# Optimization experiments

Measured on AMD Instinct MI355X. Metric: run time of the kernel, lower is better.

Reference implementation:

```python
import jax, jax.numpy as jnp
import numpy as np
from jax import lax

B, CODELEN, COMLEN, NAST, SUBG = 32, 50, 30, 300, 4
EMB, H, ASTHOPS = 300, 256, 2
AST_VOCAB, COM_VOCAB = 10000, 10000


def gru(x, h0, wih, whh, bih, bhh):
    # PyTorch GRU cell semantics. x: [N, T, D], h0: [N, H] -> (ys [N,T,H], hT [N,H])
    xg = jnp.einsum('ntd,gd->ntg', x, wih) + bih  # precompute input gates [N,T,3H]
    def step(h, xt):
        hg = h @ whh.T + bhh
        xr, xz, xn = jnp.split(xt, 3, axis=-1)
        hr, hz, hn = jnp.split(hg, 3, axis=-1)
        r = jax.nn.sigmoid(xr + hr)
        z = jax.nn.sigmoid(xz + hz)
        n = jnp.tanh(xn + r * hn)
        hnew = (1.0 - z) * n + z * h
        return hnew, hnew
    hT, ys = lax.scan(step, h0, jnp.swapaxes(xg, 0, 1))
    return jnp.swapaxes(ys, 0, 1), hT


def dot_attn(q, k):
    # DotProductAttention in eval mode (dropout = identity)
    scale = 1.0 / jnp.sqrt(jnp.asarray(q.shape[-1], q.dtype))
    s = jnp.einsum('bqd,bkd->bqk', q, k) * scale
    return jnp.einsum('bqk,bkd->bqd', jax.nn.softmax(s, axis=-1), k)


def setup_inputs() -> dict:
    key = jax.random.key(0)
    ks = jax.random.split(key, 32)
    def rn(k, shp, sc=0.05):
        return jax.random.normal(k, shp, jnp.float32) * sc
    inp = {}
    inp['x0'] = jax.random.randint(ks[0], (B, CODELEN), 0, AST_VOCAB)
    inp['x1'] = jax.random.randint(ks[1], (B, COMLEN), 0, COM_VOCAB)
    inp['x2'] = jax.random.randint(ks[2], (B, SUBG, NAST), 0, AST_VOCAB)
    inp['adj'] = jax.random.uniform(ks[3], (B, SUBG, NAST, NAST), jnp.float32) * (1.0 / NAST)
    inp['emb_ast'] = rn(ks[4], (AST_VOCAB, EMB), 0.5)
    inp['emb_com'] = rn(ks[5], (COM_VOCAB, EMB), 0.5)
    inp['gru1_wih'] = rn(ks[6], (3 * H, EMB)); inp['gru1_whh'] = rn(ks[7], (3 * H, H))
    inp['gru1_bih'] = rn(ks[8], (3 * H,));    inp['gru1_bhh'] = rn(ks[9], (3 * H,))
    inp['gru2_wih'] = rn(ks[10], (3 * H, EMB)); inp['gru2_whh'] = rn(ks[11], (3 * H, H))
    inp['gru2_bih'] = rn(ks[12], (3 * H,));     inp['gru2_bhh'] = rn(ks[13], (3 * H,))
    inp['gru4_wih'] = rn(ks[14], (3 * H, NAST * EMB), 0.01)
    inp['gru4_whh'] = rn(ks[15], (3 * H, H))
    inp['gru4_bih'] = rn(ks[16], (3 * H,)); inp['gru4_bhh'] = rn(ks[17], (3 * H,))
    inp['gru58_wih'] = rn(ks[18], (SUBG, 3 * H, EMB)); inp['gru58_whh'] = rn(ks[19], (SUBG, 3 * H, H))
    inp['gru58_bih'] = rn(ks[20], (SUBG, 3 * H));      inp['gru58_bhh'] = rn(ks[21], (SUBG, 3 * H))
    inp['gcn_w'] = rn(ks[22], (EMB, EMB)); inp['gcn_b'] = rn(ks[23], (EMB,))
    inp['dense_w'] = rn(ks[24], (H, 3 * H)); inp['dense_b'] = rn(ks[25], (H,))
    inp['lin_w'] = rn(ks[26], (COM_VOCAB, COMLEN * H), 0.01); inp['lin_b'] = rn(ks[27], (COM_VOCAB,))
    return inp


def reference(x0, x1, x2, adj, emb_ast, emb_com,
              gru1_wih, gru1_whh, gru1_bih, gru1_bhh,
              gru2_wih, gru2_whh, gru2_bih, gru2_bhh,
              gru4_wih, gru4_whh, gru4_bih, gru4_bhh,
              gru58_wih, gru58_whh, gru58_bih, gru58_bhh,
              gcn_w, gcn_b, dense_w, dense_b, lin_w, lin_b):
    b = x0.shape[0]
    scale = 1.0 / jnp.sqrt(jnp.float32(H))
    # token encoder + comment decoder
    tencout, tstate = gru(emb_ast[x0], jnp.zeros((b, H), jnp.float32),
                          gru1_wih, gru1_whh, gru1_bih, gru1_bhh)
    decout, _ = gru(emb_com[x1], tstate, gru2_wih, gru2_whh, gru2_bih, gru2_bhh)
    tcontext = dot_attn(decout, tencout)
    # GCN over 4 sub-graphs (torch code mutates astwork in place -> tmp alias sees post-GCN feats)
    astwork = jnp.transpose(emb_ast[x2], (1, 0, 2, 3))  # [4,B,N,300]
    adjp = jnp.transpose(adj, (1, 0, 2, 3))             # [4,B,N,N]
    for _ in range(ASTHOPS):
        support = jnp.einsum('sbnd,de->sbne', astwork, gcn_w)
        astwork = jax.nn.relu(jnp.einsum('sbnm,sbme->sbne', adjp, support) + gcn_b)
    # TimeDistributed(gru4): batch = 4 sub-graphs, sequence = B, input = flattened node feats
    g4in = astwork.reshape(SUBG, b, NAST * EMB)
    g4out, _ = gru(g4in, jnp.zeros((SUBG, H), jnp.float32),
                   gru4_wih, gru4_whh, gru4_bih, gru4_bhh)
    astw = jnp.transpose(g4out, (1, 0, 2))  # [B,4,H]
    ahier = jax.nn.softmax(jnp.einsum('bqd,bsd->bqs', decout, astw) * scale, axis=-1)
    ahier_p = jnp.transpose(ahier, (2, 0, 1))  # [4,B,Q]
    # per-sub-graph node GRUs (gru5..gru8) vmapped over the sub-graph axis
    outs, _ = jax.vmap(gru, in_axes=(0, None, 0, 0, 0, 0))(
        astwork, tstate, gru58_wih, gru58_whh, gru58_bih, gru58_bhh)  # [4,B,N,H]
    sc = jax.nn.softmax(jnp.einsum('bqd,sbkd->sbqk', decout, outs) * scale, axis=-1)
    new_atten = sc * ahier_p[:, :, :, None]  # element_wise_mul with hierarchy weights
    acontext = jnp.einsum('sbqk,sbkd->bqd', new_atten, outs)  # bmm then sum over sub-graphs
    acontext = dot_attn(decout, acontext)
    context = jnp.concatenate([tcontext, decout, acontext], axis=-1)  # [B,Q,768]
    out = jax.nn.relu(context @ dense_w.T + dense_b)
    out = out.reshape(b, -1)  # [B, 7680]
    return out @ lin_w.T + lin_b  # [B, comvocab]
```

## Files before the change

kernel.cpp:

```cpp
#include <hip/hip_runtime.h>
#include <hip/hip_fp16.h>
#include <hip/hip_bf16.h>


typedef __attribute__((ext_vector_type(8))) short  bf16x8;
typedef __attribute__((ext_vector_type(4))) float  f32x4;

__device__ inline unsigned short f2bs(float f) {
  __hip_bfloat16 h = __float2bfloat16(f);
  unsigned short u; __builtin_memcpy(&u, &h, 2); return u;
}
__device__ inline float bs2f(unsigned short u) {
  unsigned v = (unsigned)u << 16;
  float f; __builtin_memcpy(&f, &v, 4); return f;
}
__device__ inline float sigf(float x) { return 1.f / (1.f + __expf(-x)); }
__device__ inline float tanhf_(float x) {
  const float e = __expf(-2.f * fabsf(x));
  return copysignf((1.f - e) / (1.f + e), x);
}

template <bool ABF, bool BBF, int OUTM, bool RELU, bool GATHER = false, bool BKN = false>
__global__ __launch_bounds__(256) void k_mfma(
    const void* __restrict__ Av, long lda, long a_ss, long a_sb,
    const void* __restrict__ Bv, long ldb, long b_ss, long b_sb,
    void* __restrict__ Cv, long ldc, long c_ss, long c_sb,
    const float* __restrict__ bias, long bias_ss,
    const int* __restrict__ gidx,
    int M, int N, int K, int zb, int ksplit)
{
  __shared__ unsigned short As[128][40];
  __shared__ unsigned short Bs[128][40];
  const int tid = threadIdx.x;
  const int zi = blockIdx.z;
  const int bi = zi / ksplit;
  const int ks = zi - bi * ksplit;
  const int sIdx = bi / zb;
  const int bIdx = bi - sIdx * zb;
  const int row0 = blockIdx.y * 128;
  const int col0 = blockIdx.x * 128;
  const int Kc = ((K + ksplit * 32 - 1) / (ksplit * 32)) * 32;
  const int kbeg = ks * Kc;
  const int kend = min(K, kbeg + Kc);
  if (kbeg >= kend) return;

  const char* Ab = (const char*)Av + ((long)sIdx * a_ss + (long)bIdx * a_sb) * (ABF ? 2 : 4);
  const char* Bb = (const char*)Bv + ((long)sIdx * b_ss + (long)bIdx * b_sb) * (BBF ? 2 : 4);
  char* Cb = (char*)Cv + ((long)sIdx * c_ss + (long)bIdx * c_sb) * ((OUTM == 1 || OUTM == 3) ? 2 : 4);

  const int w = tid >> 6, l = tid & 63;
  const int wr = w >> 1, wc = w & 1;
  const int lr = l & 15, lg = l >> 4;

  f32x4 acc[4][4];
#pragma unroll
  for (int m = 0; m < 4; ++m)
#pragma unroll
    for (int n = 0; n < 4; ++n) acc[m][n] = f32x4{0.f, 0.f, 0.f, 0.f};

  const int sr = tid >> 1;
  const int sk = (tid & 1) * 16;

  for (int kt = kbeg; kt < kend; kt += 32) {
    {
      const int gr = row0 + sr;
      if (ABF) {
        const unsigned short* src = (const unsigned short*)(Ab + ((long)gr * lda + kt + sk) * 2);
        if (gr < M && kt + sk + 16 <= kend) {
          const uint2* p = (const uint2*)src;
          *(uint2*)&As[sr][sk + 0]  = p[0];
          *(uint2*)&As[sr][sk + 4]  = p[1];
          *(uint2*)&As[sr][sk + 8]  = p[2];
          *(uint2*)&As[sr][sk + 12] = p[3];
        } else {
#pragma unroll
          for (int i = 0; i < 16; ++i) {
            const int kk = kt + sk + i;
            As[sr][sk + i] = (gr < M && kk < kend) ? src[i] : (unsigned short)0;
          }
        }
      } else {
        const float* src;
        if (GATHER) src = (const float*)Av + ((gr < M) ? (long)gidx[gr] * lda : 0) + kt + sk;
        else        src = (const float*)(Ab + ((long)gr * lda + kt + sk) * 4);
        if (gr < M && kt + sk + 16 <= kend) {
#pragma unroll
          for (int q = 0; q < 4; ++q) {
            const float4 v = ((const float4*)src)[q];
            *(unsigned*)&As[sr][sk + q * 4 + 0] = (unsigned)f2bs(v.x) | ((unsigned)f2bs(v.y) << 16);
            *(unsigned*)&As[sr][sk + q * 4 + 2] = (unsigned)f2bs(v.z) | ((unsigned)f2bs(v.w) << 16);
          }
        } else {
#pragma unroll
          for (int i = 0; i < 16; ++i) {
            const int kk = kt + sk + i;
            As[sr][sk + i] = (gr < M && kk < kend) ? f2bs(src[i]) : (unsigned short)0;
          }
        }
      }
    }
    if (BKN) {
      const int kk = tid >> 3;
      const int cb = (tid & 7) * 16;
      const int gk = kt + kk;
#pragma unroll
      for (int q = 0; q < 16; ++q) {
        const int gc = col0 + cb + q;
        unsigned short v = 0;
        if (gk < kend && gc < N) {
          if (BBF) v = ((const unsigned short*)Bb)[(long)gk * ldb + gc];
          else     v = f2bs(((const float*)Bb)[(long)gk * ldb + gc]);
        }
        Bs[cb + q][kk] = v;
      }
    } else {
      const int gc = col0 + sr;
      if (BBF) {
        const unsigned short* src = (const unsigned short*)(Bb + ((long)gc * ldb + kt + sk) * 2);
        if (gc < N && kt + sk + 16 <= kend) {
          const uint2* p = (const uint2*)src;
          *(uint2*)&Bs[sr][sk + 0]  = p[0];
          *(uint2*)&Bs[sr][sk + 4]  = p[1];
          *(uint2*)&Bs[sr][sk + 8]  = p[2];
          *(uint2*)&Bs[sr][sk + 12] = p[3];
        } else {
#pragma unroll
          for (int i = 0; i < 16; ++i) {
            const int kk = kt + sk + i;
            Bs[sr][sk + i] = (gc < N && kk < kend) ? src[i] : (unsigned short)0;
          }
        }
      } else {
        const float* src = (const float*)(Bb + ((long)gc * ldb + kt + sk) * 4);
        if (gc < N && kt + sk + 16 <= kend) {
#pragma unroll
          for (int q = 0; q < 4; ++q) {
            const float4 v = ((const float4*)src)[q];
            *(unsigned*)&Bs[sr][sk + q * 4 + 0] = (unsigned)f2bs(v.x) | ((unsigned)f2bs(v.y) << 16);
            *(unsigned*)&Bs[sr][sk + q * 4 + 2] = (unsigned)f2bs(v.z) | ((unsigned)f2bs(v.w) << 16);
          }
        } else {
#pragma unroll
          for (int i = 0; i < 16; ++i) {
            const int kk = kt + sk + i;
            Bs[sr][sk + i] = (gc < N && kk < kend) ? f2bs(src[i]) : (unsigned short)0;
          }
        }
      }
    }
    __syncthreads();
    bf16x8 af[4], bf[4];
#pragma unroll
    for (int m = 0; m < 4; ++m)
      af[m] = *(const bf16x8*)&As[wr * 64 + m * 16 + lr][lg * 8];
#pragma unroll
    for (int n = 0; n < 4; ++n)
      bf[n] = *(const bf16x8*)&Bs[wc * 64 + n * 16 + lr][lg * 8];
#pragma unroll
    for (int m = 0; m < 4; ++m)
#pragma unroll
      for (int n = 0; n < 4; ++n)
        acc[m][n] = __builtin_amdgcn_mfma_f32_16x16x32_bf16(af[m], bf[n], acc[m][n], 0, 0, 0);
    __syncthreads();
  }

  const float* bp = bias ? bias + (long)sIdx * bias_ss : nullptr;
#pragma unroll
  for (int m = 0; m < 4; ++m) {
#pragma unroll
    for (int n = 0; n < 4; ++n) {
      const int col = col0 + wc * 64 + n * 16 + lr;
      const int rb  = row0 + wr * 64 + m * 16 + lg * 4;
      const f32x4 v = acc[m][n];
      if (col >= N) continue;
      if (OUTM == 3) {
        unsigned short* ct = (unsigned short*)Cb + (long)col * ldc + rb;
        if (rb + 4 <= M) {
          ushort4 pk;
          pk.x = f2bs(v[0]); pk.y = f2bs(v[1]); pk.z = f2bs(v[2]); pk.w = f2bs(v[3]);
          *(ushort4*)ct = pk;
        } else {
#pragma unroll
          for (int r = 0; r < 4; ++r) if (rb + r < M) ct[r] = f2bs(v[r]);
        }
      } else {
        const float bv = bp ? bp[col] : 0.f;
#pragma unroll
        for (int r = 0; r < 4; ++r) {
          const int row = rb + r;
          if (row >= M) continue;
          float x = v[r] + bv;
          if (RELU) x = fmaxf(x, 0.f);
          if (OUTM == 0) ((float*)Cb)[(long)row * ldc + col] = x;
          else if (OUTM == 1) ((unsigned short*)Cb)[(long)row * ldc + col] = f2bs(x);
          else atomicAdd((float*)Cb + (long)row * ldc + col, x);
        }
      }
    }
  }
}

template <int CPB, bool YBF>
__global__ __launch_bounds__(512, 2)
void k_gru_v6(
    const unsigned short* __restrict__ xg,
    const float* __restrict__ h0, int h0_mod,
    const unsigned short* __restrict__ whh_bf, long w_stride, int cpw,
    const float* __restrict__ bhh, long b_stride,
    void* __restrict__ ys, float* __restrict__ hT, int T)
{
  const int tid = threadIdx.x;
  const int c0  = blockIdx.x * CPB;
  const int wv  = tid >> 6;
  const int l   = tid & 63;
  const int lr  = l & 15;
  const int lg  = l >> 4;

  __shared__ unsigned short A_lds[512][8];
  __shared__ unsigned short w_lds[8][8][64][8];
  __shared__ float gate_lds[CPB][772];
  __shared__ float bhh_lds[768];

  const unsigned short* W = whh_bf + (long)(c0 / cpw) * w_stride;
  bf16x8 bfr[5][8];
#pragma unroll
  for (int nt = 0; nt < 5; ++nt) {
    const unsigned short* wp = W + (long)(wv * 96 + nt * 16 + lr) * 256 + lg * 8;
#pragma unroll
    for (int kt = 0; kt < 8; ++kt) bfr[nt][kt] = *(const bf16x8*)(wp + kt * 32);
  }
  {
    const unsigned short* wp = W + (long)(wv * 96 + 80 + lr) * 256 + lg * 8;
#pragma unroll
    for (int kt = 0; kt < 8; ++kt)
      *(bf16x8*)&w_lds[wv][kt][l][0] = *(const bf16x8*)(wp + kt * 32);
  }
  for (int i = tid; i < 768; i += 512)
    bhh_lds[i] = bhh[(long)(c0 / cpw) * b_stride + i];

  const bool act = lr < CPB;
  const int cO  = lr;
  const int u0  = wv * 32 + lg * 8;

  float h[8];
  {
    bf16x8 pk;
#pragma unroll
    for (int e = 0; e < 8; ++e) {
      float hv = 0.f;
      if (act && h0) hv = h0[(long)((c0 + cO) % h0_mod) * 256 + u0 + e];
      h[e] = hv;
      pk[e] = (short)f2bs(hv);
    }
    *(bf16x8*)&A_lds[tid][0] = pk;
  }

  const unsigned short* xrow = xg + (long)(c0 + cO) * T * 768 + u0;
  bf16x8 xv0, xv1, xv2;
  if (act) {
    xv0 = *(const bf16x8*)(xrow);
    xv1 = *(const bf16x8*)(xrow + 256);
    xv2 = *(const bf16x8*)(xrow + 512);
  }
  __syncthreads();

  for (int t = 0; t < T; ++t) {
    f32x4 acc[6];
#pragma unroll
    for (int nt = 0; nt < 6; ++nt) acc[nt] = f32x4{0.f, 0.f, 0.f, 0.f};
#pragma unroll
    for (int kt = 0; kt < 8; ++kt) {
      const bf16x8 af = *(const bf16x8*)&A_lds[kt * 64 + l][0];
#pragma unroll
      for (int nt = 0; nt < 5; ++nt)
        acc[nt] = __builtin_amdgcn_mfma_f32_16x16x32_bf16(af, bfr[nt][kt], acc[nt], 0, 0, 0);
      const bf16x8 wf = *(const bf16x8*)&w_lds[wv][kt][l][0];
      acc[5] = __builtin_amdgcn_mfma_f32_16x16x32_bf16(af, wf, acc[5], 0, 0, 0);
    }
    if (lg * 4 < CPB) {
#pragma unroll
      for (int nt = 0; nt < 6; ++nt) {
        const int col = wv * 96 + nt * 16 + lr;
#pragma unroll
        for (int r = 0; r < 4; ++r) gate_lds[lg * 4 + r][col] = acc[nt][r];
      }
    }
    asm volatile("s_waitcnt lgkmcnt(0)" ::: "memory");
    __builtin_amdgcn_sched_barrier(0);
    __builtin_amdgcn_s_barrier();
    __builtin_amdgcn_sched_barrier(0);

    if (act) {
      float xr[8], xz[8], xn[8];
#pragma unroll
      for (int e = 0; e < 8; ++e) {
        xr[e] = bs2f((unsigned short)xv0[e]);
        xz[e] = bs2f((unsigned short)xv1[e]);
        xn[e] = bs2f((unsigned short)xv2[e]);
      }
      bf16x8 pk;
#pragma unroll
      for (int e = 0; e < 8; ++e) {
        const int u = u0 + e;
        const float rr = sigf(xr[e] + gate_lds[cO][u] + bhh_lds[u]);
        const float zz = sigf(xz[e] + gate_lds[cO][256 + u] + bhh_lds[256 + u]);
        const float nv = tanhf_(xn[e] + rr * (gate_lds[cO][512 + u] + bhh_lds[512 + u]));
        h[e] = (1.f - zz) * nv + zz * h[e];
        pk[e] = (short)f2bs(h[e]);
      }
      *(bf16x8*)&A_lds[tid][0] = pk;
      if (YBF) {
        *(bf16x8*)((unsigned short*)ys + ((long)(c0 + cO) * T + t) * 256 + u0) = pk;
      } else {
        float* yp = (float*)ys + ((long)(c0 + cO) * T + t) * 256 + u0;
        *(float4*)yp = float4{h[0], h[1], h[2], h[3]};
        *(float4*)(yp + 4) = float4{h[4], h[5], h[6], h[7]};
      }
      if (t + 1 < T) {
        const unsigned short* xp = xrow + (long)(t + 1) * 768;
        xv0 = *(const bf16x8*)(xp);
        xv1 = *(const bf16x8*)(xp + 256);
        xv2 = *(const bf16x8*)(xp + 512);
      }
    }
    asm volatile("s_waitcnt lgkmcnt(0)" ::: "memory");
    __builtin_amdgcn_sched_barrier(0);
    __builtin_amdgcn_s_barrier();
    __builtin_amdgcn_sched_barrier(0);
  }
  if (act && hT) {
    float* hp = hT + (long)(c0 + cO) * 256 + u0;
    *(float4*)hp = float4{h[0], h[1], h[2], h[3]};
    *(float4*)(hp + 4) = float4{h[4], h[5], h[6], h[7]};
  }
}

__global__ __launch_bounds__(256) void k_init_bias(
    float* __restrict__ C, const float* __restrict__ bias, int M, int N)
{
  const int total = M * N;
  for (int i = blockIdx.x * 256 + threadIdx.x; i < total; i += gridDim.x * 256)
    C[i] = bias[i % N];
}

__global__ __launch_bounds__(256) void k_gather_ast(
    const float* __restrict__ emb, const int* __restrict__ x2,
    unsigned short* __restrict__ outp)
{
  const int total = 4 * 32 * 300 * 300;
  for (int idx = blockIdx.x * 256 + threadIdx.x; idx < total; idx += gridDim.x * 256) {
    const int d = idx % 300;
    const int r = idx / 300;
    const int n = r % 300;
    const int r2 = r / 300;
    const int b = r2 % 32;
    const int s = r2 / 32;
    outp[idx] = f2bs(emb[(long)x2[(b * 4 + s) * 300 + n] * 300 + d]);
  }
}

__global__ __launch_bounds__(256) void k_twb(
    const float* __restrict__ w, unsigned short* __restrict__ o, int R, int C)
{
  const int total = R * C;
  for (int i = blockIdx.x * 256 + threadIdx.x; i < total; i += gridDim.x * 256) {
    const int r = i / C, c = i - r * C;
    o[(long)c * R + r] = f2bs(w[i]);
  }
}

__global__ __launch_bounds__(256) void k_f2b(
    const float* __restrict__ a, unsigned short* __restrict__ o, int n)
{
  for (int i = blockIdx.x * 256 + threadIdx.x; i < n; i += gridDim.x * 256)
    o[i] = f2bs(a[i]);
}

__global__ __launch_bounds__(256) void k_attn(
    const float* __restrict__ q, const float* __restrict__ kv,
    float* __restrict__ out, int Q, int L)
{
  const int bq = blockIdx.x;
  const int b = bq / Q;
  const int tid = threadIdx.x;
  const int g = tid >> 3, l = tid & 7;
  __shared__ float qv[256];
  __shared__ float sc[64];
  qv[tid] = q[(long)bq * 256 + tid];
  __syncthreads();
  for (int k0 = 0; k0 < L; k0 += 32) {
    const int k = k0 + g;
    float s = 0.f;
    if (k < L) {
      const float* kr = kv + ((long)b * L + k) * 256;
      for (int d = l; d < 256; d += 8) s += qv[d] * kr[d];
    }
    s += __shfl_xor(s, 1);
    s += __shfl_xor(s, 2);
    s += __shfl_xor(s, 4);
    if (k < L && l == 0) sc[k] = s * 0.0625f;
  }
  __syncthreads();
  float m = -1e30f;
  for (int k = 0; k < L; ++k) m = fmaxf(m, sc[k]);
  float den = 0.f;
  for (int k = 0; k < L; ++k) den += __expf(sc[k] - m);
  __syncthreads();
  if (tid < L) sc[tid] = __expf(sc[tid] - m);
  __syncthreads();
  const float* kb = kv + (long)b * L * 256;
  float acc = 0.f;
  for (int k = 0; k < L; ++k) acc += sc[k] * kb[(long)k * 256 + tid];
  out[(long)bq * 256 + tid] = acc / den;
}

__global__ __launch_bounds__(64) void k_hier(
    const float* __restrict__ dec, const float* __restrict__ g4out,
    float* __restrict__ ahier, int Q)
{
  const int bq = blockIdx.x;
  const int b = bq / Q;
  const int l = threadIdx.x;
  float s[4] = {0.f, 0.f, 0.f, 0.f};
#pragma unroll
  for (int i = 0; i < 4; ++i) {
    const int d = l * 4 + i;
    const float qd = dec[(long)bq * 256 + d];
#pragma unroll
    for (int sg = 0; sg < 4; ++sg)
      s[sg] += qd * g4out[((long)sg * 32 + b) * 256 + d];
  }
#pragma unroll
  for (int off = 32; off >= 1; off >>= 1)
#pragma unroll
    for (int sg = 0; sg < 4; ++sg) s[sg] += __shfl_xor(s[sg], off);
  if (l == 0) {
    float m = -1e30f;
#pragma unroll
    for (int sg = 0; sg < 4; ++sg) m = fmaxf(m, s[sg] * 0.0625f);
    float e[4], den = 0.f;
#pragma unroll
    for (int sg = 0; sg < 4; ++sg) { e[sg] = __expf(s[sg] * 0.0625f - m); den += e[sg]; }
#pragma unroll
    for (int sg = 0; sg < 4; ++sg) ahier[(long)bq * 4 + sg] = e[sg] / den;
  }
}

__global__ __launch_bounds__(64) void k_smax(
    float* __restrict__ sc, const float* __restrict__ ahier)
{
  const int id = blockIdx.x;
  const int s = id / 960;
  const int bq = id - s * 960;
  float* row = sc + (long)id * 300;
  const int l = threadIdx.x;
  float v[5];
  float m = -1e30f;
#pragma unroll
  for (int i = 0; i < 5; ++i) {
    const int k = l + i * 64;
    v[i] = (k < 300) ? row[k] * 0.0625f : -1e30f;
    m = fmaxf(m, v[i]);
  }
#pragma unroll
  for (int off = 32; off >= 1; off >>= 1) m = fmaxf(m, __shfl_xor(m, off));
  float den = 0.f;
#pragma unroll
  for (int i = 0; i < 5; ++i) { v[i] = __expf(v[i] - m); den += v[i]; }
#pragma unroll
  for (int off = 32; off >= 1; off >>= 1) den += __shfl_xor(den, off);
  const float w = ahier[(long)bq * 4 + s] / den;
#pragma unroll
  for (int i = 0; i < 5; ++i) {
    const int k = l + i * 64;
    if (k < 300) row[k] = v[i] * w;
  }
}

__global__ __launch_bounds__(256) void k_concat(
    const float* __restrict__ a, const float* __restrict__ b,
    const float* __restrict__ c, float* __restrict__ out, int rows)
{
  const int total = rows * 768;
  for (int i = blockIdx.x * 256 + threadIdx.x; i < total; i += gridDim.x * 256) {
    const int r = i / 768, col = i - r * 768;
    float v;
    if (col < 256) v = a[(long)r * 256 + col];
    else if (col < 512) v = b[(long)r * 256 + col - 256];
    else v = c[(long)r * 256 + col - 512];
    out[i] = v;
  }
}

extern "C" void kernel_launch(void* const* d_in, const int* in_sizes, int n_in,
                              void* d_out, int out_size, void* d_ws, size_t ws_size,
                              hipStream_t stream) {
  const int*   x0      = (const int*)d_in[0];
  const int*   x1      = (const int*)d_in[1];
  const int*   x2      = (const int*)d_in[2];
  const float* adj     = (const float*)d_in[3];
  const float* emb_ast = (const float*)d_in[4];
  const float* emb_com = (const float*)d_in[5];
  const float* g1_wih  = (const float*)d_in[6];
  const float* g1_whh  = (const float*)d_in[7];
  const float* g1_bih  = (const float*)d_in[8];
  const float* g1_bhh  = (const float*)d_in[9];
  const float* g2_wih  = (const float*)d_in[10];
  const float* g2_whh  = (const float*)d_in[11];
  const float* g2_bih  = (const float*)d_in[12];
  const float* g2_bhh  = (const float*)d_in[13];
  const float* g4_wih  = (const float*)d_in[14];
  const float* g4_whh  = (const float*)d_in[15];
  const float* g4_bih  = (const float*)d_in[16];
  const float* g4_bhh  = (const float*)d_in[17];
  const float* g58_wih = (const float*)d_in[18];
  const float* g58_whh = (const float*)d_in[19];
  const float* g58_bih = (const float*)d_in[20];
  const float* g58_bhh = (const float*)d_in[21];
  const float* gcn_w   = (const float*)d_in[22];
  const float* gcn_b   = (const float*)d_in[23];
  const float* dw      = (const float*)d_in[24];
  const float* db      = (const float*)d_in[25];
  const float* lw      = (const float*)d_in[26];
  const float* lb      = (const float*)d_in[27];
  float* out = (float*)d_out;
  float* ws  = (float*)d_ws;

  unsigned short* astwork_bf = (unsigned short*)ws;
  unsigned short* supportT   = (unsigned short*)(ws + 5760000L);
  unsigned short* g58xg_bf   = (unsigned short*)(ws + 11520000L);
  unsigned short* outsb_bf   = (unsigned short*)(ws + 26265600L);
  unsigned short* xg1_bf     = (unsigned short*)(ws + 31180800L);
  unsigned short* xg2_bf     = (unsigned short*)(ws + 31795200L);
  float* tenc    = ws + 32163840L;
  float* tstate  = ws + 32573440L;
  float* dec     = ws + 32581632L;
  float* tctx    = ws + 32827392L;
  float* g4xg    = ws + 33073152L;
  float* g4out   = ws + 33171456L;
  float* ahier   = ws + 33204224L;
  float* actx1   = ws + 33208064L;
  float* actx    = ws + 33453824L;
  float* dense   = ws + 33699584L;
  float* ctmp    = ws + 33945344L;
  float* scbuf   = ws + 34682624L;
  unsigned short* gcn_wT    = (unsigned short*)(ws + 35834624L);
  unsigned short* dense_bf  = (unsigned short*)(ws + 35879624L);
  unsigned short* g1whh_bf  = (unsigned short*)(ws + 36002504L);
  unsigned short* g2whh_bf  = (unsigned short*)(ws + 36100808L);
  unsigned short* g4whh_bf  = (unsigned short*)(ws + 36199112L);
  unsigned short* g58whh_bf = (unsigned short*)(ws + 36297416L);
  unsigned short* adj_bf    = (unsigned short*)(ws + 36690632L);
  unsigned short* g4xg_bf   = (unsigned short*)(ws + 42450632L);

  const dim3 blk(256);

  k_gather_ast<<<dim3(4096), blk, 0, stream>>>(emb_ast, x2, astwork_bf);
  k_twb<<<dim3(90), blk, 0, stream>>>(gcn_w, gcn_wT, 300, 300);
  k_f2b<<<dim3(192), blk, 0, stream>>>(g1_whh, g1whh_bf, 196608);
  k_f2b<<<dim3(192), blk, 0, stream>>>(g2_whh, g2whh_bf, 196608);
  k_f2b<<<dim3(192), blk, 0, stream>>>(g4_whh, g4whh_bf, 196608);
  k_f2b<<<dim3(768), blk, 0, stream>>>(g58_whh, g58whh_bf, 786432);
  k_f2b<<<dim3(4096), blk, 0, stream>>>(adj, adj_bf, 11520000);

  for (int hop = 0; hop < 2; ++hop) {
    k_mfma<true, true, 3, false><<<dim3(3, 3, 128), blk, 0, stream>>>(
        astwork_bf, 300, 2880000, 90000,
        gcn_wT, 300, 0, 0,
        supportT, 300, 2880000, 90000,
        nullptr, 0, nullptr, 300, 300, 300, 32, 1);
    k_mfma<true, true, 1, true><<<dim3(3, 3, 128), blk, 0, stream>>>(
        adj_bf, 300, 90000, 360000,
        supportT, 300, 2880000, 90000,
        astwork_bf, 300, 2880000, 90000,
        gcn_b, 0, nullptr, 300, 300, 300, 32, 1);
  }

  k_mfma<false, false, 1, false, true><<<dim3(6, 13, 1), blk, 0, stream>>>(
      emb_ast, 300, 0, 0, g1_wih, 300, 0, 0, xg1_bf, 768, 0, 0,
      g1_bih, 0, x0, 1600, 768, 300, 1, 1);
  k_gru_v6<8, false><<<dim3(4), dim3(512), 0, stream>>>(
      xg1_bf, nullptr, 1, g1whh_bf, 0, 32, g1_bhh, 0, tenc, tstate, 50);

  k_mfma<false, false, 1, false, true><<<dim3(6, 8, 1), blk, 0, stream>>>(
      emb_com, 300, 0, 0, g2_wih, 300, 0, 0, xg2_bf, 768, 0, 0,
      g2_bih, 0, x1, 960, 768, 300, 1, 1);
  k_gru_v6<8, false><<<dim3(4), dim3(512), 0, stream>>>(
      xg2_bf, tstate, 32, g2whh_bf, 0, 32, g2_bhh, 0, dec, nullptr, 30);

  k_attn<<<dim3(960), blk, 0, stream>>>(dec, tenc, tctx, 30, 50);

  k_init_bias<<<dim3(384), blk, 0, stream>>>(g4xg, g4_bih, 128, 768);
  k_mfma<true, false, 2, false><<<dim3(6, 1, 43), blk, 0, stream>>>(
      astwork_bf, 90000, 0, 0, g4_wih, 90000, 0, 0, g4xg, 768, 0, 0,
      nullptr, 0, nullptr, 128, 768, 90000, 1, 43);
  k_f2b<<<dim3(384), blk, 0, stream>>>(g4xg, g4xg_bf, 98304);
  k_gru_v6<4, false><<<dim3(1), dim3(512), 0, stream>>>(
      g4xg_bf, nullptr, 1, g4whh_bf, 0, 4, g4_bhh, 0, g4out, nullptr, 32);

  k_hier<<<dim3(960), dim3(64), 0, stream>>>(dec, g4out, ahier, 30);

  k_mfma<true, false, 1, false><<<dim3(6, 75, 4), blk, 0, stream>>>(
      astwork_bf, 300, 2880000, 0, g58_wih, 300, 230400, 0,
      g58xg_bf, 768, 7372800, 0, g58_bih, 768, nullptr, 9600, 768, 300, 1, 1);
  k_gru_v6<8, true><<<dim3(16), dim3(512), 0, stream>>>(
      g58xg_bf, tstate, 32, g58whh_bf, 196608, 32, g58_bhh, 768,
      outsb_bf, nullptr, 300);

  k_mfma<false, true, 0, false><<<dim3(3, 1, 128), blk, 0, stream>>>(
      dec, 256, 0, 7680, outsb_bf, 256, 2457600, 76800, scbuf, 300, 288000, 9000,
      nullptr, 0, nullptr, 30, 300, 256, 32, 1);
  k_smax<<<dim3(3840), dim3(64), 0, stream>>>(scbuf, ahier);
  hipMemsetAsync(actx1, 0, 245760 * sizeof(float), stream);
  k_mfma<false, true, 2, false, false, true><<<dim3(2, 1, 128), blk, 0, stream>>>(
      scbuf, 300, 288000, 9000, outsb_bf, 256, 2457600, 76800, actx1, 256, 0, 7680,
      nullptr, 0, nullptr, 30, 256, 300, 32, 1);

  k_attn<<<dim3(960), blk, 0, stream>>>(dec, actx1, actx, 30, 30);

  k_concat<<<dim3(2880), blk, 0, stream>>>(tctx, dec, actx, ctmp, 960);
  k_mfma<false, false, 0, true><<<dim3(2, 8, 1), blk, 0, stream>>>(
      ctmp, 768, 0, 0, dw, 768, 0, 0, dense, 256, 0, 0,
      db, 0, nullptr, 960, 256, 768, 1, 1);
  k_f2b<<<dim3(960), blk, 0, stream>>>(dense, dense_bf, 245760);

  k_init_bias<<<dim3(1250), blk, 0, stream>>>(out, lb, 32, 10000);
  k_mfma<true, false, 2, false><<<dim3(79, 1, 6), blk, 0, stream>>>(
      dense_bf, 7680, 0, 0, lw, 7680, 0, 0, out, 10000, 0, 0,
      nullptr, 0, nullptr, 32, 10000, 7680, 1, 6);
}
```

Measured before the change: 2.104 ms.

## Replace MFMA batched GRU with one-sequence-per-block fp16 register GRU

Replaces the GRU recurrence kernel, which batched 8 sequences per block with MFMA and bf16 weights, with one sequence per 1024-thread block. Each thread keeps its share of the fp16-packed recurrent weights in registers and computes dot products with packed half2 FMAs, then reduces across 4 lanes with shuffles. This spreads the serial recurrences over many more CUs (128 blocks for the 300-step sub-graph GRU) and drops the separate weight-conversion kernels. The cost is fp16 accumulation in short partial sums, which loses some precision, and heavy register pressure from 96 half2 weight registers per thread.

```diff
diff --git a/kernel.cpp b/kernel.cpp
--- a/kernel.cpp
+++ b/kernel.cpp
@@ -200,139 +200,101 @@
   }
 }
 
-template <int CPB, bool YBF>
-__global__ __launch_bounds__(512, 2)
-void k_gru_v6(
+template <bool YBF>
+__global__ __launch_bounds__(1024) void k_gru_v7(
     const unsigned short* __restrict__ xg,
     const float* __restrict__ h0, int h0_mod,
-    const unsigned short* __restrict__ whh_bf, long w_stride, int cpw,
+    const float* __restrict__ whh, long w_stride, int cpw,
     const float* __restrict__ bhh, long b_stride,
     void* __restrict__ ys, float* __restrict__ hT, int T)
 {
+  const int c   = blockIdx.x;
   const int tid = threadIdx.x;
-  const int c0  = blockIdx.x * CPB;
-  const int wv  = tid >> 6;
-  const int l   = tid & 63;
-  const int lr  = l & 15;
-  const int lg  = l >> 4;
-
-  __shared__ unsigned short A_lds[512][8];
-  __shared__ unsigned short w_lds[8][8][64][8];
-  __shared__ float gate_lds[CPB][772];
-  __shared__ float bhh_lds[768];
-
-  const unsigned short* W = whh_bf + (long)(c0 / cpw) * w_stride;
-  bf16x8 bfr[5][8];
-#pragma unroll
-  for (int nt = 0; nt < 5; ++nt) {
-    const unsigned short* wp = W + (long)(wv * 96 + nt * 16 + lr) * 256 + lg * 8;
-#pragma unroll
-    for (int kt = 0; kt < 8; ++kt) bfr[nt][kt] = *(const bf16x8*)(wp + kt * 32);
-  }
+  const int j   = tid >> 2;
+  const int kq  = tid & 3;
+
+  __shared__ __half h16[256];
+
+  const float* W = whh + (long)(c / cpw) * w_stride;
+  __half2 wr[32], wz[32], wn[32];
   {
-    const unsigned short* wp = W + (long)(wv * 96 + 80 + lr) * 256 + lg * 8;
-#pragma unroll
-    for (int kt = 0; kt < 8; ++kt)
-      *(bf16x8*)&w_lds[wv][kt][l][0] = *(const bf16x8*)(wp + kt * 32);
-  }
-  for (int i = tid; i < 768; i += 512)
-    bhh_lds[i] = bhh[(long)(c0 / cpw) * b_stride + i];
-
-  const bool act = lr < CPB;
-  const int cO  = lr;
-  const int u0  = wv * 32 + lg * 8;
-
-  float h[8];
-  {
-    bf16x8 pk;
-#pragma unroll
-    for (int e = 0; e < 8; ++e) {
-      float hv = 0.f;
-      if (act && h0) hv = h0[(long)((c0 + cO) % h0_mod) * 256 + u0 + e];
-      h[e] = hv;
-      pk[e] = (short)f2bs(hv);
-    }
-    *(bf16x8*)&A_lds[tid][0] = pk;
-  }
-
-  const unsigned short* xrow = xg + (long)(c0 + cO) * T * 768 + u0;
-  bf16x8 xv0, xv1, xv2;
+    const float* pr = W + (long)j * 256 + kq * 64;
+    const float* pz = W + (long)(j + 256) * 256 + kq * 64;
+    const float* pn = W + (long)(j + 512) * 256 + kq * 64;
+#pragma unroll
+    for (int i = 0; i < 32; ++i) {
+      wr[i] = __floats2half2_rn(pr[2 * i], pr[2 * i + 1]);
+      wz[i] = __floats2half2_rn(pz[2 * i], pz[2 * i + 1]);
+      wn[i] = __floats2half2_rn(pn[2 * i], pn[2 * i + 1]);
+    }
+  }
+
+  const bool act = (kq == 0);
+  float br = 0.f, bz = 0.f, bn = 0.f, hold = 0.f;
   if (act) {
-    xv0 = *(const bf16x8*)(xrow);
-    xv1 = *(const bf16x8*)(xrow + 256);
-    xv2 = *(const bf16x8*)(xrow + 512);
-  }
-  __syncthreads();
+    const float* Bh = bhh + (long)(c / cpw) * b_stride;
+    br = Bh[j]; bz = Bh[256 + j]; bn = Bh[512 + j];
+    hold = h0 ? h0[(long)(c % h0_mod) * 256 + j] : 0.f;
+    h16[j] = __float2half(hold);
+  }
+  const unsigned short* xrow = xg + (long)c * T * 768;
+  float xr = 0.f, xz = 0.f, xn = 0.f;
+  if (act) {
+    xr = bs2f(xrow[j]); xz = bs2f(xrow[256 + j]); xn = bs2f(xrow[512 + j]);
+  }
+  asm volatile("s_waitcnt lgkmcnt(0)" ::: "memory");
+  __builtin_amdgcn_sched_barrier(0);
+  __builtin_amdgcn_s_barrier();
+  __builtin_amdgcn_sched_barrier(0);
 
   for (int t = 0; t < T; ++t) {
-    f32x4 acc[6];
-#pragma unroll
-    for (int nt = 0; nt < 6; ++nt) acc[nt] = f32x4{0.f, 0.f, 0.f, 0.f};
-#pragma unroll
-    for (int kt = 0; kt < 8; ++kt) {
-      const bf16x8 af = *(const bf16x8*)&A_lds[kt * 64 + l][0];
-#pragma unroll
-      for (int nt = 0; nt < 5; ++nt)
-        acc[nt] = __builtin_amdgcn_mfma_f32_16x16x32_bf16(af, bfr[nt][kt], acc[nt], 0, 0, 0);
-      const bf16x8 wf = *(const bf16x8*)&w_lds[wv][kt][l][0];
-      acc[5] = __builtin_amdgcn_mfma_f32_16x16x32_bf16(af, wf, acc[5], 0, 0, 0);
-    }
-    if (lg * 4 < CPB) {
-#pragma unroll
-      for (int nt = 0; nt < 6; ++nt) {
-        const int col = wv * 96 + nt * 16 + lr;
-#pragma unroll
-        for (int r = 0; r < 4; ++r) gate_lds[lg * 4 + r][col] = acc[nt][r];
+    float nxr = 0.f, nxz = 0.f, nxn = 0.f;
+    if (act && t + 1 < T) {
+      const unsigned short* xp = xrow + (long)(t + 1) * 768;
+      nxr = bs2f(xp[j]); nxz = bs2f(xp[256 + j]); nxn = bs2f(xp[512 + j]);
+    }
+    const __half2* hp = (const __half2*)&h16[0] + kq * 32;
+    float sr = 0.f, sz = 0.f, sn = 0.f;
+#pragma unroll
+    for (int i0 = 0; i0 < 32; i0 += 8) {
+      __half2 ar = __float2half2_rn(0.f);
+      __half2 az = __float2half2_rn(0.f);
+      __half2 an = __float2half2_rn(0.f);
+#pragma unroll
+      for (int i = 0; i < 8; ++i) {
+        const __half2 hv = hp[i0 + i];
+        ar = __hfma2(wr[i0 + i], hv, ar);
+        az = __hfma2(wz[i0 + i], hv, az);
+        an = __hfma2(wn[i0 + i], hv, an);
       }
-    }
+      sr += __low2float(ar) + __high2float(ar);
+      sz += __low2float(az) + __high2float(az);
+      sn += __low2float(an) + __high2float(an);
+    }
+    sr += __shfl_xor(sr, 1); sr += __shfl_xor(sr, 2);
+    sz += __shfl_xor(sz, 1); sz += __shfl_xor(sz, 2);
+    sn += __shfl_xor(sn, 1); sn += __shfl_xor(sn, 2);
     asm volatile("s_waitcnt lgkmcnt(0)" ::: "memory");
     __builtin_amdgcn_sched_barrier(0);
     __builtin_amdgcn_s_barrier();
     __builtin_amdgcn_sched_barrier(0);
 
     if (act) {
-      float xr[8], xz[8], xn[8];
-#pragma unroll
-      for (int e = 0; e < 8; ++e) {
-        xr[e] = bs2f((unsigned short)xv0[e]);
-        xz[e] = bs2f((unsigned short)xv1[e]);
-        xn[e] = bs2f((unsigned short)xv2[e]);
-      }
-      bf16x8 pk;
-#pragma unroll
-      for (int e = 0; e < 8; ++e) {
-        const int u = u0 + e;
-        const float rr = sigf(xr[e] + gate_lds[cO][u] + bhh_lds[u]);
-        const float zz = sigf(xz[e] + gate_lds[cO][256 + u] + bhh_lds[256 + u]);
-        const float nv = tanhf_(xn[e] + rr * (gate_lds[cO][512 + u] + bhh_lds[512 + u]));
-        h[e] = (1.f - zz) * nv + zz * h[e];
-        pk[e] = (short)f2bs(h[e]);
-      }
-      *(bf16x8*)&A_lds[tid][0] = pk;
-      if (YBF) {
-        *(bf16x8*)((unsigned short*)ys + ((long)(c0 + cO) * T + t) * 256 + u0) = pk;
-      } else {
-        float* yp = (float*)ys + ((long)(c0 + cO) * T + t) * 256 + u0;
-        *(float4*)yp = float4{h[0], h[1], h[2], h[3]};
-        *(float4*)(yp + 4) = float4{h[4], h[5], h[6], h[7]};
-      }
-      if (t + 1 < T) {
-        const unsigned short* xp = xrow + (long)(t + 1) * 768;
-        xv0 = *(const bf16x8*)(xp);
-        xv1 = *(const bf16x8*)(xp + 256);
-        xv2 = *(const bf16x8*)(xp + 512);
-      }
-    }
+      const float rr = sigf(xr + sr + br);
+      const float zz = sigf(xz + sz + bz);
+      const float nv = tanhf_(xn + rr * (sn + bn));
+      hold = (1.f - zz) * nv + zz * hold;
+      h16[j] = __float2half(hold);
+      if (YBF) ((unsigned short*)ys)[((long)c * T + t) * 256 + j] = f2bs(hold);
+      else     ((float*)ys)[((long)c * T + t) * 256 + j] = hold;
+    }
+    xr = nxr; xz = nxz; xn = nxn;
     asm volatile("s_waitcnt lgkmcnt(0)" ::: "memory");
     __builtin_amdgcn_sched_barrier(0);
     __builtin_amdgcn_s_barrier();
     __builtin_amdgcn_sched_barrier(0);
   }
-  if (act && hT) {
-    float* hp = hT + (long)(c0 + cO) * 256 + u0;
-    *(float4*)hp = float4{h[0], h[1], h[2], h[3]};
-    *(float4*)(hp + 4) = float4{h[4], h[5], h[6], h[7]};
-  }
+  if (act && hT) hT[(long)c * 256 + j] = hold;
 }
 
 __global__ __launch_bounds__(256) void k_init_bias(
@@ -546,10 +508,6 @@
   float* scbuf   = ws + 34682624L;
   unsigned short* gcn_wT    = (unsigned short*)(ws + 35834624L);
   unsigned short* dense_bf  = (unsigned short*)(ws + 35879624L);
-  unsigned short* g1whh_bf  = (unsigned short*)(ws + 36002504L);
-  unsigned short* g2whh_bf  = (unsigned short*)(ws + 36100808L);
-  unsigned short* g4whh_bf  = (unsigned short*)(ws + 36199112L);
-  unsigned short* g58whh_bf = (unsigned short*)(ws + 36297416L);
   unsigned short* adj_bf    = (unsigned short*)(ws + 36690632L);
   unsigned short* g4xg_bf   = (unsigned short*)(ws + 42450632L);
 
@@ -557,10 +515,6 @@
 
   k_gather_ast<<<dim3(4096), blk, 0, stream>>>(emb_ast, x2, astwork_bf);
   k_twb<<<dim3(90), blk, 0, stream>>>(gcn_w, gcn_wT, 300, 300);
-  k_f2b<<<dim3(192), blk, 0, stream>>>(g1_whh, g1whh_bf, 196608);
-  k_f2b<<<dim3(192), blk, 0, stream>>>(g2_whh, g2whh_bf, 196608);
-  k_f2b<<<dim3(192), blk, 0, stream>>>(g4_whh, g4whh_bf, 196608);
-  k_f2b<<<dim3(768), blk, 0, stream>>>(g58_whh, g58whh_bf, 786432);
   k_f2b<<<dim3(4096), blk, 0, stream>>>(adj, adj_bf, 11520000);
 
   for (int hop = 0; hop < 2; ++hop) {
@@ -579,14 +533,14 @@
   k_mfma<false, false, 1, false, true><<<dim3(6, 13, 1), blk, 0, stream>>>(
       emb_ast, 300, 0, 0, g1_wih, 300, 0, 0, xg1_bf, 768, 0, 0,
       g1_bih, 0, x0, 1600, 768, 300, 1, 1);
-  k_gru_v6<8, false><<<dim3(4), dim3(512), 0, stream>>>(
-      xg1_bf, nullptr, 1, g1whh_bf, 0, 32, g1_bhh, 0, tenc, tstate, 50);
+  k_gru_v7<false><<<dim3(32), dim3(1024), 0, stream>>>(
+      xg1_bf, nullptr, 1, g1_whh, 0, 32, g1_bhh, 0, tenc, tstate, 50);
 
   k_mfma<false, false, 1, false, true><<<dim3(6, 8, 1), blk, 0, stream>>>(
       emb_com, 300, 0, 0, g2_wih, 300, 0, 0, xg2_bf, 768, 0, 0,
       g2_bih, 0, x1, 960, 768, 300, 1, 1);
-  k_gru_v6<8, false><<<dim3(4), dim3(512), 0, stream>>>(
-      xg2_bf, tstate, 32, g2whh_bf, 0, 32, g2_bhh, 0, dec, nullptr, 30);
+  k_gru_v7<false><<<dim3(32), dim3(1024), 0, stream>>>(
+      xg2_bf, tstate, 32, g2_whh, 0, 32, g2_bhh, 0, dec, nullptr, 30);
 
   k_attn<<<dim3(960), blk, 0, stream>>>(dec, tenc, tctx, 30, 50);
 
@@ -595,16 +549,16 @@
       astwork_bf, 90000, 0, 0, g4_wih, 90000, 0, 0, g4xg, 768, 0, 0,
       nullptr, 0, nullptr, 128, 768, 90000, 1, 43);
   k_f2b<<<dim3(384), blk, 0, stream>>>(g4xg, g4xg_bf, 98304);
-  k_gru_v6<4, false><<<dim3(1), dim3(512), 0, stream>>>(
-      g4xg_bf, nullptr, 1, g4whh_bf, 0, 4, g4_bhh, 0, g4out, nullptr, 32);
+  k_gru_v7<false><<<dim3(4), dim3(1024), 0, stream>>>(
+      g4xg_bf, nullptr, 1, g4_whh, 0, 4, g4_bhh, 0, g4out, nullptr, 32);
 
   k_hier<<<dim3(960), dim3(64), 0, stream>>>(dec, g4out, ahier, 30);
 
   k_mfma<true, false, 1, false><<<dim3(6, 75, 4), blk, 0, stream>>>(
       astwork_bf, 300, 2880000, 0, g58_wih, 300, 230400, 0,
       g58xg_bf, 768, 7372800, 0, g58_bih, 768, nullptr, 9600, 768, 300, 1, 1);
-  k_gru_v6<8, true><<<dim3(16), dim3(512), 0, stream>>>(
-      g58xg_bf, tstate, 32, g58whh_bf, 196608, 32, g58_bhh, 768,
+  k_gru_v7<true><<<dim3(128), dim3(1024), 0, stream>>>(
+      g58xg_bf, tstate, 32, g58_whh, 196608, 32, g58_bhh, 768,
       outsb_bf, nullptr, 300);
 
   k_mfma<false, true, 0, false><<<dim3(3, 1, 128), blk, 0, stream>>>(
```

Measured after the change: 1.929 ms. 8.3% less time.
